# Performance work log

Measured on AMD Instinct MI355X. Metric: run time of the kernel, lower is better.

Reference implementation:

```python
import jax, jax.numpy as jnp
import numpy as np

N = 50000
E = 800000
NUM_KINDS = 100
D_NODE = 64
D_EDGE = 4
D_MSG = 64
L = 3
D_IN = 2 * D_NODE + D_EDGE  # 132


def setup_inputs() -> dict:
    key = jax.random.key(0)
    ks = jax.random.split(key, 20)

    def w(k, shape, fan_in):
        bound = 1.0 / np.sqrt(fan_in)
        return jax.random.uniform(k, shape, jnp.float32, -bound, bound)

    inp = {
        "edge_index": jax.random.randint(ks[0], (2, E), 0, N),
        "node_kind_ids": jax.random.randint(ks[1], (N,), 0, NUM_KINDS),
        "edge_attr": jax.random.normal(ks[2], (E, D_EDGE), jnp.float32),
        # learned params
        "emb": jax.random.normal(ks[3], (NUM_KINDS, D_NODE), jnp.float32),
        # stacked per-layer message MLP params [L, ...]
        "msg_w1": w(ks[4], (L, D_MSG, D_IN), D_IN),
        "msg_b1": w(ks[5], (L, D_MSG), D_IN),
        "msg_w2": w(ks[6], (L, D_MSG, D_MSG), D_MSG),
        "msg_b2": w(ks[7], (L, D_MSG), D_MSG),
        # stacked per-layer GRUCell params (torch layout: [3*d_node, d_in])
        "gru_wih": w(ks[8], (L, 3 * D_NODE, D_MSG), D_NODE),
        "gru_whh": w(ks[9], (L, 3 * D_NODE, D_NODE), D_NODE),
        "gru_bih": w(ks[10], (L, 3 * D_NODE), D_NODE),
        "gru_bhh": w(ks[11], (L, 3 * D_NODE), D_NODE),
        # edge head: Linear(132,64) -> SiLU -> Linear(64,1)
        "head_w1": w(ks[12], (64, D_IN), D_IN),
        "head_b1": w(ks[13], (64,), D_IN),
        "head_w2": w(ks[14], (1, 64), 64),
        "head_b2": w(ks[15], (1,), 64),
    }
    return inp


def reference(edge_index, node_kind_ids, edge_attr, emb,
              msg_w1, msg_b1, msg_w2, msg_b2,
              gru_wih, gru_whh, gru_bih, gru_bhh,
              head_w1, head_b1, head_w2, head_b2):
    src, dst = edge_index[0], edge_index[1]
    h = emb[node_kind_ids]  # [N, d_node]
    n_nodes = h.shape[0]
    for l in range(L):
        x = jnp.concatenate([h[src], h[dst], edge_attr], axis=1)  # [E, 132]
        m = jax.nn.silu(x @ msg_w1[l].T + msg_b1[l]) @ msg_w2[l].T + msg_b2[l]  # [E, d_msg]
        agg = jax.ops.segment_sum(m, dst, num_segments=n_nodes)  # [N, d_msg]
        # torch GRUCell math
        gi = agg @ gru_wih[l].T + gru_bih[l]  # [N, 3*d_node]
        gh = h @ gru_whh[l].T + gru_bhh[l]
        ir, iz, inn = jnp.split(gi, 3, axis=1)
        hr, hz, hn = jnp.split(gh, 3, axis=1)
        r = jax.nn.sigmoid(ir + hr)
        z = jax.nn.sigmoid(iz + hz)
        n = jnp.tanh(inn + r * hn)
        h = (1.0 - z) * n + z * h
    x = jnp.concatenate([h[src], h[dst], edge_attr], axis=1)  # [E, 132]
    logits = (jax.nn.silu(x @ head_w1.T + head_b1) @ head_w2.T + head_b2)[:, 0]
    return jax.nn.sigmoid(logits)  # [E]
```

## Files before the change

### kernel.cpp

```cpp
#include <hip/hip_runtime.h>
#include <hip/hip_bf16.h>


typedef __attribute__((ext_vector_type(8))) short bf16x8;
typedef __attribute__((ext_vector_type(4))) float f32x4;
#define MFMA16(a, b, c) __builtin_amdgcn_mfma_f32_16x16x32_bf16(a, b, c, 0, 0, 0)

#define CHUNK 128
#define XSTRIDE 336
#define MSTRIDE 264
#define HSTRIDE 144
#define SLABSZ 10752
#define HIDSZ  4608

#define WRZST 264
#define WNST  136

__device__ __forceinline__ float fast_sig(float x) { return 1.f / (1.f + __expf(-x)); }
__device__ __forceinline__ float fast_tanh(float x) {
    float ax = fabsf(x);
    float t = __expf(-2.f * ax);
    return copysignf((1.f - t) / (1.f + t), x);
}
__device__ __forceinline__ ushort f2bf(float f) {
    unsigned u = __float_as_uint(f);
    unsigned r = u + 0x7FFF + ((u >> 16) & 1);
    return (ushort)(r >> 16);
}

__global__ void prep_kernel(const float* __restrict__ msg_w1,
                            const float* __restrict__ msg_w2,
                            const float* __restrict__ gru_wih,
                            const float* __restrict__ gru_whh,
                            const float* __restrict__ head_w1,
                            const float* __restrict__ head_w2,
                            ushort* __restrict__ Wb1, ushort* __restrict__ Wb2,
                            ushort* __restrict__ Wh1, ushort* __restrict__ Wh2b,
                            ushort* __restrict__ Wrz, ushort* __restrict__ Wni,
                            ushort* __restrict__ Wnh) {
    int t = blockIdx.x * 256 + threadIdx.x;
    if (t < 30720) {
        int l = t / 10240, r = t % 10240, j = r / 160, k = r % 160;
        Wb1[t] = (k < 132) ? f2bf(msg_w1[l * 8448 + j * 132 + k]) : 0;
        return;
    }
    t -= 30720;
    if (t < 12288) {
        Wb2[t] = f2bf(msg_w2[t]);
        return;
    }
    t -= 12288;
    if (t < 10240) {
        int j = t / 160, k = t % 160;
        Wh1[t] = (k < 132) ? f2bf(head_w1[j * 132 + k]) : 0;
        return;
    }
    t -= 10240;
    if (t < 1024) {
        int j = t >> 6, k = t & 63;
        Wh2b[t] = (j == 0) ? f2bf(head_w2[k]) : 0;
        return;
    }
    t -= 1024;
    if (t < 49152) {
        int l = t / 16384, r = t % 16384, n = r >> 7, k = r & 127;
        float v = (k < 64) ? gru_wih[l * 12288 + n * 64 + k]
                           : gru_whh[l * 12288 + n * 64 + (k - 64)];
        Wrz[t] = f2bf(v);
        return;
    }
    t -= 49152;
    if (t < 12288) {
        int l = t / 4096, r = t % 4096, j = r >> 6, k = r & 63;
        Wni[t] = f2bf(gru_wih[l * 12288 + (128 + j) * 64 + k]);
        return;
    }
    t -= 12288;
    if (t < 12288) {
        int l = t / 4096, r = t % 4096, j = r >> 6, k = r & 63;
        Wnh[t] = f2bf(gru_whh[l * 12288 + (128 + j) * 64 + k]);
    }
}

__global__ void embed_kernel(float* __restrict__ h, ushort* __restrict__ hb,
                             const float* __restrict__ emb,
                             const int* __restrict__ kinds, int N) {
    int t = blockIdx.x * 256 + threadIdx.x;
    if (t >= N * 64) return;
    int node = t >> 6, d = t & 63;
    float v = emb[kinds[node] * 64 + d];
    h[t] = v;
    hb[t] = f2bf(v);
}

__global__ void hist_kernel(const int* __restrict__ dst, int* __restrict__ deg, int E) {
    int e = blockIdx.x * 256 + threadIdx.x;
    if (e < E) atomicAdd(&deg[dst[e]], 1);
}

__global__ void scan_kernel(const int* __restrict__ deg, int* __restrict__ cursor, int N) {
    __shared__ int sums[1024];
    int tid = threadIdx.x;
    int chunk = (N + 1023) >> 10;
    int lo = tid * chunk, hi = min(lo + chunk, N);
    int s = 0;
    for (int i = lo; i < hi; i++) s += deg[i];
    sums[tid] = s;
    __syncthreads();
    for (int off = 1; off < 1024; off <<= 1) {
        int v = (tid >= off) ? sums[tid - off] : 0;
        __syncthreads();
        sums[tid] += v;
        __syncthreads();
    }
    int run = (tid > 0) ? sums[tid - 1] : 0;
    for (int i = lo; i < hi; i++) {
        cursor[i] = run;
        run += deg[i];
    }
}

__global__ void scatter_kernel(const int* __restrict__ src, const int* __restrict__ dst,
                               const float* __restrict__ ea, int* __restrict__ cursor,
                               int* __restrict__ src_s, int* __restrict__ dst_s,
                               ushort* __restrict__ ea_sb, int E) {
    int e = blockIdx.x * 256 + threadIdx.x;
    if (e >= E) return;
    int d = dst[e];
    int p = atomicAdd(&cursor[d], 1);
    src_s[p] = src[e];
    dst_s[p] = d;
    float4 e4 = ((const float4*)ea)[e];
    ushort4 eb;
    eb.x = f2bf(e4.x); eb.y = f2bf(e4.y); eb.z = f2bf(e4.z); eb.w = f2bf(e4.w);
    ((ushort4*)ea_sb)[p] = eb;
}

__global__ __launch_bounds__(256) void edge_msg_mfma(
    const ushort* __restrict__ hb, const int* __restrict__ src_s,
    const int* __restrict__ dst_s, const ushort* __restrict__ ea_sb,
    const ushort* __restrict__ Wb1l, const ushort* __restrict__ Wb2l,
    const float* __restrict__ b1, const float* __restrict__ b2,
    float* __restrict__ agg, int E, int nchunks) {
    __shared__ char lds[4 * SLABSZ + 4 * HIDSZ];
    int tid = threadIdx.x;
    int w = tid >> 6, lane = tid & 63;
    int quad = lane >> 4, nrow = lane & 15;
    char* slab = lds + w * SLABSZ;
    char* hidb = lds + 4 * SLABSZ + w * HIDSZ;

    bf16x8 wf1[4][5], wf2[4][2];
    float b1v[4], b2v[4];
#pragma unroll
    for (int nt = 0; nt < 4; nt++) {
        int n = nt * 16 + nrow;
#pragma unroll
        for (int ks = 0; ks < 5; ks++)
            wf1[nt][ks] = *(const bf16x8*)(Wb1l + n * 160 + ks * 32 + quad * 8);
#pragma unroll
        for (int ks = 0; ks < 2; ks++)
            wf2[nt][ks] = *(const bf16x8*)(Wb2l + n * 64 + ks * 32 + quad * 8);
        b1v[nt] = b1[n];
        b2v[nt] = b2[n];
    }

    for (int chunk = blockIdx.x; chunk < nchunks; chunk += gridDim.x) {
        int ebase = chunk * CHUNK;
        {
            int el = tid >> 1, half = tid & 1;
            int r = el & 31;
            int ec = min(ebase + el, E - 1);
            int node = half ? dst_s[ec] : src_s[ec];
            const float4* hrow = (const float4*)(hb + (size_t)node * 64);
            float4* xw = (float4*)(slab + r * XSTRIDE + half * 128);
#pragma unroll
            for (int i = 0; i < 8; i++) xw[i] = hrow[i];
            if (half == 0) {
                *(uint2*)(slab + r * XSTRIDE + 256) = *(const uint2*)(ea_sb + (size_t)ec * 4);
            } else {
                uint2 z2 = {0u, 0u};
                float4 z4 = {0.f, 0.f, 0.f, 0.f};
                *(uint2*)(slab + r * XSTRIDE + 264) = z2;
                *(float4*)(slab + r * XSTRIDE + 272) = z4;
                *(float4*)(slab + r * XSTRIDE + 288) = z4;
                *(float4*)(slab + r * XSTRIDE + 304) = z4;
            }
        }
        f32x4 acc1[2][4];
#pragma unroll
        for (int mt = 0; mt < 2; mt++)
#pragma unroll
            for (int nt = 0; nt < 4; nt++) {
                f32x4 v;
                v[0] = v[1] = v[2] = v[3] = b1v[nt];
                acc1[mt][nt] = v;
            }
#pragma unroll
        for (int ks = 0; ks < 5; ks++) {
            bf16x8 a0 = *(const bf16x8*)(slab + nrow * XSTRIDE + ks * 64 + quad * 16);
            bf16x8 a1 = *(const bf16x8*)(slab + (16 + nrow) * XSTRIDE + ks * 64 + quad * 16);
#pragma unroll
            for (int nt = 0; nt < 4; nt++) {
                acc1[0][nt] = MFMA16(a0, wf1[nt][ks], acc1[0][nt]);
                acc1[1][nt] = MFMA16(a1, wf1[nt][ks], acc1[1][nt]);
            }
        }
#pragma unroll
        for (int mt = 0; mt < 2; mt++)
#pragma unroll
            for (int nt = 0; nt < 4; nt++)
#pragma unroll
                for (int rg = 0; rg < 4; rg++) {
                    float v = acc1[mt][nt][rg];
                    v = v * fast_sig(v);
                    int rm = mt * 16 + quad * 4 + rg;
                    *(ushort*)(hidb + rm * HSTRIDE + (nt * 16 + nrow) * 2) = f2bf(v);
                }
        f32x4 acc2[2][4];
#pragma unroll
        for (int mt = 0; mt < 2; mt++)
#pragma unroll
            for (int nt = 0; nt < 4; nt++) {
                f32x4 v;
                v[0] = v[1] = v[2] = v[3] = b2v[nt];
                acc2[mt][nt] = v;
            }
#pragma unroll
        for (int ks = 0; ks < 2; ks++) {
            bf16x8 a0 = *(const bf16x8*)(hidb + nrow * HSTRIDE + ks * 64 + quad * 16);
            bf16x8 a1 = *(const bf16x8*)(hidb + (16 + nrow) * HSTRIDE + ks * 64 + quad * 16);
#pragma unroll
            for (int nt = 0; nt < 4; nt++) {
                acc2[0][nt] = MFMA16(a0, wf2[nt][ks], acc2[0][nt]);
                acc2[1][nt] = MFMA16(a1, wf2[nt][ks], acc2[1][nt]);
            }
        }
#pragma unroll
        for (int mt = 0; mt < 2; mt++)
#pragma unroll
            for (int nt = 0; nt < 4; nt++)
#pragma unroll
                for (int rg = 0; rg < 4; rg++) {
                    int rm = mt * 16 + quad * 4 + rg;
                    *(float*)(slab + rm * MSTRIDE + (nt * 16 + nrow) * 4) = acc2[mt][nt][rg];
                }
        {
            int e32 = ebase + w * 32;
            int dmy = dst_s[min(e32 + (lane & 31), E - 1)];
            int limit = min(32, E - e32);
            int nx = __shfl_down(dmy, 1);
            bool tl = ((lane & 31) == 31) || (dmy != nx);
            unsigned long long tm = __ballot(tl);
            float run = 0.f;
#pragma unroll
            for (int i = 0; i < 32; i++) {
                if (i < limit) {
                    run += *(const float*)(slab + i * MSTRIDE + lane * 4);
                    if (((tm >> i) & 1ull) || (i + 1 == limit)) {
                        int di = __shfl(dmy, i);
                        unsafeAtomicAdd(&agg[(size_t)di * 64 + lane], run);
                        run = 0.f;
                    }
                }
            }
        }
    }
}

__global__ __launch_bounds__(256) void head_mfma(
    const ushort* __restrict__ hb, const int* __restrict__ src,
    const int* __restrict__ dst, const float* __restrict__ ea,
    const ushort* __restrict__ Wh1, const ushort* __restrict__ Wh2b,
    const float* __restrict__ hb1, const float* __restrict__ hb2p,
    float* __restrict__ out, int E, int nchunks) {
    __shared__ char lds[4 * SLABSZ + 4 * HIDSZ];
    int tid = threadIdx.x;
    int w = tid >> 6, lane = tid & 63;
    int quad = lane >> 4, nrow = lane & 15;
    char* slab = lds + w * SLABSZ;
    char* hidb = lds + 4 * SLABSZ + w * HIDSZ;

    bf16x8 wf1[4][5], wh2[2];
    float b1v[4];
#pragma unroll
    for (int nt = 0; nt < 4; nt++) {
        int n = nt * 16 + nrow;
#pragma unroll
        for (int ks = 0; ks < 5; ks++)
            wf1[nt][ks] = *(const bf16x8*)(Wh1 + n * 160 + ks * 32 + quad * 8);
        b1v[nt] = hb1[n];
    }
#pragma unroll
    for (int ks = 0; ks < 2; ks++)
        wh2[ks] = *(const bf16x8*)(Wh2b + nrow * 64 + ks * 32 + quad * 8);
    float hb2 = hb2p[0];

    for (int chunk = blockIdx.x; chunk < nchunks; chunk += gridDim.x) {
        int ebase = chunk * CHUNK;
        {
            int el = tid >> 1, half = tid & 1;
            int r = el & 31;
            int ec = min(ebase + el, E - 1);
            int node = half ? dst[ec] : src[ec];
            const float4* hrow = (const float4*)(hb + (size_t)node * 64);
            float4* xw = (float4*)(slab + r * XSTRIDE + half * 128);
#pragma unroll
            for (int i = 0; i < 8; i++) xw[i] = hrow[i];
            if (half == 0) {
                float4 e4 = ((const float4*)ea)[ec];
                ushort4 eb;
                eb.x = f2bf(e4.x); eb.y = f2bf(e4.y); eb.z = f2bf(e4.z); eb.w = f2bf(e4.w);
                *(ushort4*)(slab + r * XSTRIDE + 256) = eb;
            } else {
                uint2 z2 = {0u, 0u};
                float4 z4 = {0.f, 0.f, 0.f, 0.f};
                *(uint2*)(slab + r * XSTRIDE + 264) = z2;
                *(float4*)(slab + r * XSTRIDE + 272) = z4;
                *(float4*)(slab + r * XSTRIDE + 288) = z4;
                *(float4*)(slab + r * XSTRIDE + 304) = z4;
            }
        }
        f32x4 acc1[2][4];
#pragma unroll
        for (int mt = 0; mt < 2; mt++)
#pragma unroll
            for (int nt = 0; nt < 4; nt++) {
                f32x4 v;
                v[0] = v[1] = v[2] = v[3] = b1v[nt];
                acc1[mt][nt] = v;
            }
#pragma unroll
        for (int ks = 0; ks < 5; ks++) {
            bf16x8 a0 = *(const bf16x8*)(slab + nrow * XSTRIDE + ks * 64 + quad * 16);
            bf16x8 a1 = *(const bf16x8*)(slab + (16 + nrow) * XSTRIDE + ks * 64 + quad * 16);
#pragma unroll
            for (int nt = 0; nt < 4; nt++) {
                acc1[0][nt] = MFMA16(a0, wf1[nt][ks], acc1[0][nt]);
                acc1[1][nt] = MFMA16(a1, wf1[nt][ks], acc1[1][nt]);
            }
        }
#pragma unroll
        for (int mt = 0; mt < 2; mt++)
#pragma unroll
            for (int nt = 0; nt < 4; nt++)
#pragma unroll
                for (int rg = 0; rg < 4; rg++) {
                    float v = acc1[mt][nt][rg];
                    v = v * fast_sig(v);
                    int rm = mt * 16 + quad * 4 + rg;
                    *(ushort*)(hidb + rm * HSTRIDE + (nt * 16 + nrow) * 2) = f2bf(v);
                }
        f32x4 acc3[2];
#pragma unroll
        for (int mt = 0; mt < 2; mt++) {
            f32x4 v;
            v[0] = v[1] = v[2] = v[3] = 0.f;
            acc3[mt] = v;
        }
#pragma unroll
        for (int ks = 0; ks < 2; ks++) {
            bf16x8 a0 = *(const bf16x8*)(hidb + nrow * HSTRIDE + ks * 64 + quad * 16);
            bf16x8 a1 = *(const bf16x8*)(hidb + (16 + nrow) * HSTRIDE + ks * 64 + quad * 16);
            acc3[0] = MFMA16(a0, wh2[ks], acc3[0]);
            acc3[1] = MFMA16(a1, wh2[ks], acc3[1]);
        }
        if (nrow == 0) {
#pragma unroll
            for (int mt = 0; mt < 2; mt++)
#pragma unroll
                for (int rg = 0; rg < 4; rg++) {
                    int e = ebase + w * 32 + mt * 16 + quad * 4 + rg;
                    if (e < E) out[e] = fast_sig(acc3[mt][rg] + hb2);
                }
        }
    }
}

__device__ __forceinline__ bf16x8 aggfrag(const float* __restrict__ row, int off) {
    float4 f0 = *(const float4*)(row + off);
    float4 f1 = *(const float4*)(row + off + 4);
    bf16x8 r;
    r[0] = (short)f2bf(f0.x); r[1] = (short)f2bf(f0.y);
    r[2] = (short)f2bf(f0.z); r[3] = (short)f2bf(f0.w);
    r[4] = (short)f2bf(f1.x); r[5] = (short)f2bf(f1.y);
    r[6] = (short)f2bf(f1.z); r[7] = (short)f2bf(f1.w);
    return r;
}

__global__ __launch_bounds__(256) void gru_mfma(
    float* __restrict__ h, ushort* __restrict__ hb, const float* __restrict__ agg,
    const ushort* __restrict__ Wrzg, const ushort* __restrict__ Wnig,
    const ushort* __restrict__ Wnhg,
    const float* __restrict__ bih, const float* __restrict__ bhh, int N) {
    __shared__ char lds[128 * WRZST + 2 * 64 * WNST];
    int tid = threadIdx.x, w = tid >> 6, lane = tid & 63;
    int quad = lane >> 4, nrow = lane & 15;
    char* wrz = lds;
    char* wni = lds + 128 * WRZST;
    char* wnh = wni + 64 * WNST;

    {
        int r = tid >> 1, half = tid & 1;
        const uint4* g = (const uint4*)(Wrzg + r * 128 + half * 64);
        uint4* d = (uint4*)(wrz + r * WRZST + half * 128);
#pragma unroll
        for (int i = 0; i < 8; i++) d[i] = g[i];
        if (tid < 128) {
            const uint4* g2 = (const uint4*)(Wnig + (tid >> 1) * 64 + (tid & 1) * 32);
            uint4* d2 = (uint4*)(wni + (tid >> 1) * WNST + (tid & 1) * 64);
#pragma unroll
            for (int i = 0; i < 4; i++) d2[i] = g2[i];
        } else {
            int t2 = tid - 128;
            const uint4* g2 = (const uint4*)(Wnhg + (t2 >> 1) * 64 + (t2 & 1) * 32);
            uint4* d2 = (uint4*)(wnh + (t2 >> 1) * WNST + (t2 & 1) * 64);
#pragma unroll
            for (int i = 0; i < 4; i++) d2[i] = g2[i];
        }
    }
    __syncthreads();

    int nb0 = blockIdx.x * 128 + w * 32;
    if (nb0 >= N) return;

    float brz[8], bi[4], bhv[4];
#pragma unroll
    for (int nt = 0; nt < 8; nt++) brz[nt] = bih[nt * 16 + nrow] + bhh[nt * 16 + nrow];
#pragma unroll
    for (int nt = 0; nt < 4; nt++) {
        bi[nt] = bih[128 + nt * 16 + nrow];
        bhv[nt] = bhh[128 + nt * 16 + nrow];
    }

    int n0 = min(nb0 + nrow, N - 1);
    int n1 = min(nb0 + 16 + nrow, N - 1);
    const float* ag0 = agg + (size_t)n0 * 64;
    const float* ag1 = agg + (size_t)n1 * 64;
    const ushort* hb0 = hb + (size_t)n0 * 64;
    const ushort* hb1 = hb + (size_t)n1 * 64;

    f32x4 accrz[2][8], acci[2][4], acch[2][4];
#pragma unroll
    for (int nt = 0; nt < 8; nt++) {
        f32x4 v; v[0] = v[1] = v[2] = v[3] = brz[nt];
        accrz[0][nt] = v; accrz[1][nt] = v;
    }
#pragma unroll
    for (int nt = 0; nt < 4; nt++) {
        f32x4 vi; vi[0] = vi[1] = vi[2] = vi[3] = bi[nt];
        acci[0][nt] = vi; acci[1][nt] = vi;
        f32x4 vh; vh[0] = vh[1] = vh[2] = vh[3] = bhv[nt];
        acch[0][nt] = vh; acch[1][nt] = vh;
    }

#pragma unroll
    for (int ks = 0; ks < 4; ks++) {
        bf16x8 a0, a1;
        if (ks < 2) {
            a0 = aggfrag(ag0, ks * 32 + quad * 8);
            a1 = aggfrag(ag1, ks * 32 + quad * 8);
        } else {
            a0 = *(const bf16x8*)(hb0 + (ks - 2) * 32 + quad * 8);
            a1 = *(const bf16x8*)(hb1 + (ks - 2) * 32 + quad * 8);
        }
#pragma unroll
        for (int nt = 0; nt < 8; nt++) {
            bf16x8 b = *(const bf16x8*)(wrz + (nt * 16 + nrow) * WRZST + ks * 64 + quad * 16);
            accrz[0][nt] = MFMA16(a0, b, accrz[0][nt]);
            accrz[1][nt] = MFMA16(a1, b, accrz[1][nt]);
        }
        if (ks < 2) {
#pragma unroll
            for (int nt = 0; nt < 4; nt++) {
                bf16x8 b = *(const bf16x8*)(wni + (nt * 16 + nrow) * WNST + ks * 64 + quad * 16);
                acci[0][nt] = MFMA16(a0, b, acci[0][nt]);
                acci[1][nt] = MFMA16(a1, b, acci[1][nt]);
            }
        } else {
#pragma unroll
            for (int nt = 0; nt < 4; nt++) {
                bf16x8 b = *(const bf16x8*)(wnh + (nt * 16 + nrow) * WNST + (ks - 2) * 64 + quad * 16);
                acch[0][nt] = MFMA16(a0, b, acch[0][nt]);
                acch[1][nt] = MFMA16(a1, b, acch[1][nt]);
            }
        }
    }

#pragma unroll
    for (int mt = 0; mt < 2; mt++)
#pragma unroll
        for (int nt = 0; nt < 4; nt++)
#pragma unroll
            for (int rg = 0; rg < 4; rg++) {
                int node = nb0 + mt * 16 + quad * 4 + rg;
                if (node < N) {
                    int col = nt * 16 + nrow;
                    float r = fast_sig(accrz[mt][nt][rg]);
                    float z = fast_sig(accrz[mt][nt + 4][rg]);
                    float nn = fast_tanh(acci[mt][nt][rg] + r * acch[mt][nt][rg]);
                    size_t idx = (size_t)node * 64 + col;
                    float ho = h[idx];
                    float hnew = (1.f - z) * nn + z * ho;
                    h[idx] = hnew;
                    hb[idx] = f2bf(hnew);
                }
            }
}

extern "C" void kernel_launch(void* const* d_in, const int* in_sizes, int n_in,
                              void* d_out, int out_size, void* d_ws, size_t ws_size,
                              hipStream_t stream) {
    const int* edge_index = (const int*)d_in[0];
    int E = in_sizes[0] / 2;
    const int* src = edge_index;
    const int* dst = edge_index + E;
    const int* kinds = (const int*)d_in[1];
    int N = in_sizes[1];
    const float* edge_attr = (const float*)d_in[2];
    const float* emb = (const float*)d_in[3];
    const float* msg_w1 = (const float*)d_in[4];
    const float* msg_b1 = (const float*)d_in[5];
    const float* msg_w2 = (const float*)d_in[6];
    const float* msg_b2 = (const float*)d_in[7];
    const float* gru_wih = (const float*)d_in[8];
    const float* gru_whh = (const float*)d_in[9];
    const float* gru_bih = (const float*)d_in[10];
    const float* gru_bhh = (const float*)d_in[11];
    const float* head_w1 = (const float*)d_in[12];
    const float* head_b1 = (const float*)d_in[13];
    const float* head_w2 = (const float*)d_in[14];
    const float* head_b2 = (const float*)d_in[15];
    float* out = (float*)d_out;

    char* p = (char*)d_ws;
    float* h = (float*)p;        p += (size_t)N * 64 * 4;
    float* agg = (float*)p;      p += (size_t)N * 64 * 4;
    int* deg = (int*)p;          p += (size_t)N * 4;
    int* cursor = (int*)p;       p += (size_t)N * 4;
    int* src_s = (int*)p;        p += (size_t)E * 4;
    int* dst_s = (int*)p;        p += (size_t)E * 4;
    ushort* hb = (ushort*)p;     p += (size_t)N * 64 * 2;
    ushort* Wb1 = (ushort*)p;    p += 30720 * 2;
    ushort* Wb2 = (ushort*)p;    p += 12288 * 2;
    ushort* Wh1 = (ushort*)p;    p += 10240 * 2;
    ushort* Wh2b = (ushort*)p;   p += 1024 * 2;
    ushort* Wrz = (ushort*)p;    p += 49152 * 2;
    ushort* Wni = (ushort*)p;    p += 12288 * 2;
    ushort* Wnh = (ushort*)p;    p += 12288 * 2;
    ushort* ea_sb = (ushort*)p;  p += (size_t)E * 4 * 2;

    int nchunks = (E + CHUNK - 1) / CHUNK;

    prep_kernel<<<500, 256, 0, stream>>>(msg_w1, msg_w2, gru_wih, gru_whh, head_w1,
                                         head_w2, Wb1, Wb2, Wh1, Wh2b, Wrz, Wni, Wnh);
    embed_kernel<<<(N * 64 + 255) / 256, 256, 0, stream>>>(h, hb, emb, kinds, N);

    hipMemsetAsync(deg, 0, (size_t)N * sizeof(int), stream);
    hist_kernel<<<(E + 255) / 256, 256, 0, stream>>>(dst, deg, E);
    scan_kernel<<<1, 1024, 0, stream>>>(deg, cursor, N);
    scatter_kernel<<<(E + 255) / 256, 256, 0, stream>>>(src, dst, edge_attr, cursor,
                                                        src_s, dst_s, ea_sb, E);

    for (int l = 0; l < 3; l++) {
        hipMemsetAsync(agg, 0, (size_t)N * 64 * sizeof(float), stream);
        edge_msg_mfma<<<512, 256, 0, stream>>>(
            hb, src_s, dst_s, ea_sb,
            Wb1 + l * 10240, Wb2 + l * 4096,
            msg_b1 + l * 64, msg_b2 + l * 64, agg, E, nchunks);
        gru_mfma<<<(N + 127) / 128, 256, 0, stream>>>(
            h, hb, agg, Wrz + l * 16384, Wni + l * 4096, Wnh + l * 4096,
            gru_bih + l * 192, gru_bhh + l * 192, N);
    }
    head_mfma<<<512, 256, 0, stream>>>(hb, src, dst, edge_attr, Wh1, Wh2b,
                                       head_b1, head_b2, out, E, nchunks);
}
```

Measured before the change: 686.3 us.

## Load gathered node rows directly into MFMA registers, skipping the LDS staging slab

The edge message and head kernels now gather h[src]/h[dst] rows and edge attributes straight into MFMA operand registers, using the transposed product (W as A, X as B), instead of staging a padded slab in LDS. The hidden activations go to a smaller XOR-swizzled LDS buffer and are packed to bf16 with v_cvt_pk_bf16_f32. LDS use per block shrinks, which should let more blocks run per CU. The segmented atomic reduction is split into groups of 8 rows, which may issue more atomics.

```diff
diff --git a/kernel.cpp b/kernel.cpp
--- a/kernel.cpp
+++ b/kernel.cpp
@@ -7,11 +7,9 @@
 #define MFMA16(a, b, c) __builtin_amdgcn_mfma_f32_16x16x32_bf16(a, b, c, 0, 0, 0)
 
 #define CHUNK 128
-#define XSTRIDE 336
 #define MSTRIDE 264
-#define HSTRIDE 144
-#define SLABSZ 10752
-#define HIDSZ  4608
+#define EBUF 8448
+#define HIDB 4096
 
 #define WRZST 264
 #define WNST  136
@@ -26,6 +24,11 @@
     unsigned u = __float_as_uint(f);
     unsigned r = u + 0x7FFF + ((u >> 16) & 1);
     return (ushort)(r >> 16);
+}
+__device__ __forceinline__ unsigned pkbf2(float a, float b) {
+    unsigned r;
+    asm("v_cvt_pk_bf16_f32 %0, %1, %2" : "=v"(r) : "v"(a), "v"(b));
+    return r;
 }
 
 __global__ void prep_kernel(const float* __restrict__ msg_w1,
@@ -142,15 +145,15 @@
     const ushort* __restrict__ Wb1l, const ushort* __restrict__ Wb2l,
     const float* __restrict__ b1, const float* __restrict__ b2,
     float* __restrict__ agg, int E, int nchunks) {
-    __shared__ char lds[4 * SLABSZ + 4 * HIDSZ];
+    __shared__ char lds[4 * EBUF];
     int tid = threadIdx.x;
     int w = tid >> 6, lane = tid & 63;
     int quad = lane >> 4, nrow = lane & 15;
-    char* slab = lds + w * SLABSZ;
-    char* hidb = lds + 4 * SLABSZ + w * HIDSZ;
+    char* buf = lds + w * EBUF;
 
     bf16x8 wf1[4][5], wf2[4][2];
-    float b1v[4], b2v[4];
+    f32x4 b1q[4];
+    float b2v[4];
 #pragma unroll
     for (int nt = 0; nt < 4; nt++) {
         int n = nt * 16 + nrow;
@@ -160,81 +163,100 @@
 #pragma unroll
         for (int ks = 0; ks < 2; ks++)
             wf2[nt][ks] = *(const bf16x8*)(Wb2l + n * 64 + ks * 32 + quad * 8);
-        b1v[nt] = b1[n];
+        b1q[nt] = *(const f32x4*)(b1 + nt * 16 + quad * 4);
         b2v[nt] = b2[n];
     }
 
     for (int chunk = blockIdx.x; chunk < nchunks; chunk += gridDim.x) {
-        int ebase = chunk * CHUNK;
+        int ebase = chunk * CHUNK + w * 32;
+        int e0 = min(ebase + nrow, E - 1);
+        int e1 = min(ebase + 16 + nrow, E - 1);
+        int s0 = src_s[e0], s1 = src_s[e1];
+        int d0 = dst_s[e0], d1 = dst_s[e1];
+
+        bf16x8 x0[5], x1[5];
         {
-            int el = tid >> 1, half = tid & 1;
-            int r = el & 31;
-            int ec = min(ebase + el, E - 1);
-            int node = half ? dst_s[ec] : src_s[ec];
-            const float4* hrow = (const float4*)(hb + (size_t)node * 64);
-            float4* xw = (float4*)(slab + r * XSTRIDE + half * 128);
-#pragma unroll
-            for (int i = 0; i < 8; i++) xw[i] = hrow[i];
-            if (half == 0) {
-                *(uint2*)(slab + r * XSTRIDE + 256) = *(const uint2*)(ea_sb + (size_t)ec * 4);
-            } else {
-                uint2 z2 = {0u, 0u};
-                float4 z4 = {0.f, 0.f, 0.f, 0.f};
-                *(uint2*)(slab + r * XSTRIDE + 264) = z2;
-                *(float4*)(slab + r * XSTRIDE + 272) = z4;
-                *(float4*)(slab + r * XSTRIDE + 288) = z4;
-                *(float4*)(slab + r * XSTRIDE + 304) = z4;
-            }
-        }
-        f32x4 acc1[2][4];
+            const ushort* p = hb + (size_t)s0 * 64 + quad * 8;
+            x0[0] = *(const bf16x8*)p;
+            x0[1] = *(const bf16x8*)(p + 32);
+            p = hb + (size_t)d0 * 64 + quad * 8;
+            x0[2] = *(const bf16x8*)p;
+            x0[3] = *(const bf16x8*)(p + 32);
+            p = hb + (size_t)s1 * 64 + quad * 8;
+            x1[0] = *(const bf16x8*)p;
+            x1[1] = *(const bf16x8*)(p + 32);
+            p = hb + (size_t)d1 * 64 + quad * 8;
+            x1[2] = *(const bf16x8*)p;
+            x1[3] = *(const bf16x8*)(p + 32);
+            bf16x8 z = {0, 0, 0, 0, 0, 0, 0, 0};
+            x0[4] = z;
+            x1[4] = z;
+            if (quad == 0) {
+                ushort4 v0 = *(const ushort4*)(ea_sb + (size_t)e0 * 4);
+                ushort4 v1 = *(const ushort4*)(ea_sb + (size_t)e1 * 4);
+                x0[4][0] = (short)v0.x; x0[4][1] = (short)v0.y;
+                x0[4][2] = (short)v0.z; x0[4][3] = (short)v0.w;
+                x1[4][0] = (short)v1.x; x1[4][1] = (short)v1.y;
+                x1[4][2] = (short)v1.z; x1[4][3] = (short)v1.w;
+            }
+        }
+
+        f32x4 acc[4][2];
+#pragma unroll
+        for (int nt = 0; nt < 4; nt++) {
+            acc[nt][0] = b1q[nt];
+            acc[nt][1] = b1q[nt];
+        }
+#pragma unroll
+        for (int ks = 0; ks < 5; ks++)
+#pragma unroll
+            for (int nt = 0; nt < 4; nt++) {
+                acc[nt][0] = MFMA16(wf1[nt][ks], x0[ks], acc[nt][0]);
+                acc[nt][1] = MFMA16(wf1[nt][ks], x1[ks], acc[nt][1]);
+            }
+
+#pragma unroll
+        for (int nt = 0; nt < 4; nt++)
+#pragma unroll
+            for (int et = 0; et < 2; et++) {
+                f32x4 a = acc[nt][et];
+                float v0 = a[0] * fast_sig(a[0]);
+                float v1 = a[1] * fast_sig(a[1]);
+                float v2 = a[2] * fast_sig(a[2]);
+                float v3 = a[3] * fast_sig(a[3]);
+                int er = et * 16 + nrow;
+                int off = er * 128 + ((nt * 32 + quad * 8) ^ ((er & 7) << 4));
+                uint2 pk;
+                pk.x = pkbf2(v0, v1);
+                pk.y = pkbf2(v2, v3);
+                *(uint2*)(buf + off) = pk;
+            }
+
+        bf16x8 ha[2][2];
 #pragma unroll
         for (int mt = 0; mt < 2; mt++)
 #pragma unroll
+            for (int ks = 0; ks < 2; ks++) {
+                int er = mt * 16 + nrow;
+                ha[mt][ks] = *(const bf16x8*)(
+                    buf + er * 128 + ((ks * 64 + quad * 16) ^ ((er & 7) << 4)));
+            }
+        f32x4 acc2[2][4];
+#pragma unroll
+        for (int nt = 0; nt < 4; nt++) {
+            f32x4 v;
+            v[0] = v[1] = v[2] = v[3] = b2v[nt];
+            acc2[0][nt] = v;
+            acc2[1][nt] = v;
+        }
+#pragma unroll
+        for (int ks = 0; ks < 2; ks++)
+#pragma unroll
             for (int nt = 0; nt < 4; nt++) {
-                f32x4 v;
-                v[0] = v[1] = v[2] = v[3] = b1v[nt];
-                acc1[mt][nt] = v;
-            }
-#pragma unroll
-        for (int ks = 0; ks < 5; ks++) {
-            bf16x8 a0 = *(const bf16x8*)(slab + nrow * XSTRIDE + ks * 64 + quad * 16);
-            bf16x8 a1 = *(const bf16x8*)(slab + (16 + nrow) * XSTRIDE + ks * 64 + quad * 16);
-#pragma unroll
-            for (int nt = 0; nt < 4; nt++) {
-                acc1[0][nt] = MFMA16(a0, wf1[nt][ks], acc1[0][nt]);
-                acc1[1][nt] = MFMA16(a1, wf1[nt][ks], acc1[1][nt]);
-            }
-        }
-#pragma unroll
-        for (int mt = 0; mt < 2; mt++)
-#pragma unroll
-            for (int nt = 0; nt < 4; nt++)
-#pragma unroll
-                for (int rg = 0; rg < 4; rg++) {
-                    float v = acc1[mt][nt][rg];
-                    v = v * fast_sig(v);
-                    int rm = mt * 16 + quad * 4 + rg;
-                    *(ushort*)(hidb + rm * HSTRIDE + (nt * 16 + nrow) * 2) = f2bf(v);
-                }
-        f32x4 acc2[2][4];
-#pragma unroll
-        for (int mt = 0; mt < 2; mt++)
-#pragma unroll
-            for (int nt = 0; nt < 4; nt++) {
-                f32x4 v;
-                v[0] = v[1] = v[2] = v[3] = b2v[nt];
-                acc2[mt][nt] = v;
-            }
-#pragma unroll
-        for (int ks = 0; ks < 2; ks++) {
-            bf16x8 a0 = *(const bf16x8*)(hidb + nrow * HSTRIDE + ks * 64 + quad * 16);
-            bf16x8 a1 = *(const bf16x8*)(hidb + (16 + nrow) * HSTRIDE + ks * 64 + quad * 16);
-#pragma unroll
-            for (int nt = 0; nt < 4; nt++) {
-                acc2[0][nt] = MFMA16(a0, wf2[nt][ks], acc2[0][nt]);
-                acc2[1][nt] = MFMA16(a1, wf2[nt][ks], acc2[1][nt]);
-            }
-        }
+                acc2[0][nt] = MFMA16(ha[0][ks], wf2[nt][ks], acc2[0][nt]);
+                acc2[1][nt] = MFMA16(ha[1][ks], wf2[nt][ks], acc2[1][nt]);
+            }
+
 #pragma unroll
         for (int mt = 0; mt < 2; mt++)
 #pragma unroll
@@ -242,24 +264,29 @@
 #pragma unroll
                 for (int rg = 0; rg < 4; rg++) {
                     int rm = mt * 16 + quad * 4 + rg;
-                    *(float*)(slab + rm * MSTRIDE + (nt * 16 + nrow) * 4) = acc2[mt][nt][rg];
+                    *(float*)(buf + rm * MSTRIDE + (nt * 16 + nrow) * 4) =
+                        acc2[mt][nt][rg];
                 }
+
         {
-            int e32 = ebase + w * 32;
-            int dmy = dst_s[min(e32 + (lane & 31), E - 1)];
-            int limit = min(32, E - e32);
+            int dmy = (lane & 16) ? d1 : d0;
+            int limit = min(32, E - ebase);
             int nx = __shfl_down(dmy, 1);
             bool tl = ((lane & 31) == 31) || (dmy != nx);
             unsigned long long tm = __ballot(tl);
-            float run = 0.f;
-#pragma unroll
-            for (int i = 0; i < 32; i++) {
-                if (i < limit) {
-                    run += *(const float*)(slab + i * MSTRIDE + lane * 4);
-                    if (((tm >> i) & 1ull) || (i + 1 == limit)) {
-                        int di = __shfl(dmy, i);
-                        unsafeAtomicAdd(&agg[(size_t)di * 64 + lane], run);
-                        run = 0.f;
+#pragma unroll
+            for (int g = 0; g < 4; g++) {
+                float run = 0.f;
+#pragma unroll
+                for (int i = 0; i < 8; i++) {
+                    int idx = g * 8 + i;
+                    if (idx < limit) {
+                        run += *(const float*)(buf + idx * MSTRIDE + lane * 4);
+                        if (((tm >> idx) & 1ull) || (i == 7) || (idx + 1 == limit)) {
+                            int di = __shfl(dmy, idx);
+                            unsafeAtomicAdd(&agg[(size_t)di * 64 + lane], run);
+                            run = 0.f;
+                        }
                     }
                 }
             }
@@ -273,22 +300,21 @@
     const ushort* __restrict__ Wh1, const ushort* __restrict__ Wh2b,
     const float* __restrict__ hb1, const float* __restrict__ hb2p,
     float* __restrict__ out, int E, int nchunks) {
-    __shared__ char lds[4 * SLABSZ + 4 * HIDSZ];
+    __shared__ char lds[4 * HIDB];
     int tid = threadIdx.x;
     int w = tid >> 6, lane = tid & 63;
     int quad = lane >> 4, nrow = lane & 15;
-    char* slab = lds + w * SLABSZ;
-    char* hidb = lds + 4 * SLABSZ + w * HIDSZ;
+    char* buf = lds + w * HIDB;
 
     bf16x8 wf1[4][5], wh2[2];
-    float b1v[4];
+    f32x4 b1q[4];
 #pragma unroll
     for (int nt = 0; nt < 4; nt++) {
         int n = nt * 16 + nrow;
 #pragma unroll
         for (int ks = 0; ks < 5; ks++)
             wf1[nt][ks] = *(const bf16x8*)(Wh1 + n * 160 + ks * 32 + quad * 8);
-        b1v[nt] = hb1[n];
+        b1q[nt] = *(const f32x4*)(hb1 + nt * 16 + quad * 4);
     }
 #pragma unroll
     for (int ks = 0; ks < 2; ks++)
@@ -296,60 +322,79 @@
     float hb2 = hb2p[0];
 
     for (int chunk = blockIdx.x; chunk < nchunks; chunk += gridDim.x) {
-        int ebase = chunk * CHUNK;
+        int ebase = chunk * CHUNK + w * 32;
+        int e0 = min(ebase + nrow, E - 1);
+        int e1 = min(ebase + 16 + nrow, E - 1);
+        int s0 = src[e0], s1 = src[e1];
+        int d0 = dst[e0], d1 = dst[e1];
+
+        bf16x8 x0[5], x1[5];
         {
-            int el = tid >> 1, half = tid & 1;
-            int r = el & 31;
-            int ec = min(ebase + el, E - 1);
-            int node = half ? dst[ec] : src[ec];
-            const float4* hrow = (const float4*)(hb + (size_t)node * 64);
-            float4* xw = (float4*)(slab + r * XSTRIDE + half * 128);
-#pragma unroll
-            for (int i = 0; i < 8; i++) xw[i] = hrow[i];
-            if (half == 0) {
-                float4 e4 = ((const float4*)ea)[ec];
-                ushort4 eb;
-                eb.x = f2bf(e4.x); eb.y = f2bf(e4.y); eb.z = f2bf(e4.z); eb.w = f2bf(e4.w);
-                *(ushort4*)(slab + r * XSTRIDE + 256) = eb;
-            } else {
-                uint2 z2 = {0u, 0u};
-                float4 z4 = {0.f, 0.f, 0.f, 0.f};
-                *(uint2*)(slab + r * XSTRIDE + 264) = z2;
-                *(float4*)(slab + r * XSTRIDE + 272) = z4;
-                *(float4*)(slab + r * XSTRIDE + 288) = z4;
-                *(float4*)(slab + r * XSTRIDE + 304) = z4;
-            }
-        }
-        f32x4 acc1[2][4];
+            const ushort* p = hb + (size_t)s0 * 64 + quad * 8;
+            x0[0] = *(const bf16x8*)p;
+            x0[1] = *(const bf16x8*)(p + 32);
+            p = hb + (size_t)d0 * 64 + quad * 8;
+            x0[2] = *(const bf16x8*)p;
+            x0[3] = *(const bf16x8*)(p + 32);
+            p = hb + (size_t)s1 * 64 + quad * 8;
+            x1[0] = *(const bf16x8*)p;
+            x1[1] = *(const bf16x8*)(p + 32);
+            p = hb + (size_t)d1 * 64 + quad * 8;
+            x1[2] = *(const bf16x8*)p;
+            x1[3] = *(const bf16x8*)(p + 32);
+            bf16x8 z = {0, 0, 0, 0, 0, 0, 0, 0};
+            x0[4] = z;
+            x1[4] = z;
+            if (quad == 0) {
+                float4 q0 = ((const float4*)ea)[e0];
+                float4 q1 = ((const float4*)ea)[e1];
+                x0[4][0] = (short)f2bf(q0.x); x0[4][1] = (short)f2bf(q0.y);
+                x0[4][2] = (short)f2bf(q0.z); x0[4][3] = (short)f2bf(q0.w);
+                x1[4][0] = (short)f2bf(q1.x); x1[4][1] = (short)f2bf(q1.y);
+                x1[4][2] = (short)f2bf(q1.z); x1[4][3] = (short)f2bf(q1.w);
+            }
+        }
+
+        f32x4 acc[4][2];
+#pragma unroll
+        for (int nt = 0; nt < 4; nt++) {
+            acc[nt][0] = b1q[nt];
+            acc[nt][1] = b1q[nt];
+        }
+#pragma unroll
+        for (int ks = 0; ks < 5; ks++)
+#pragma unroll
+            for (int nt = 0; nt < 4; nt++) {
+                acc[nt][0] = MFMA16(wf1[nt][ks], x0[ks], acc[nt][0]);
+                acc[nt][1] = MFMA16(wf1[nt][ks], x1[ks], acc[nt][1]);
+            }
+
+#pragma unroll
+        for (int nt = 0; nt < 4; nt++)
+#pragma unroll
+            for (int et = 0; et < 2; et++) {
+                f32x4 a = acc[nt][et];
+                float v0 = a[0] * fast_sig(a[0]);
+                float v1 = a[1] * fast_sig(a[1]);
+                float v2 = a[2] * fast_sig(a[2]);
+                float v3 = a[3] * fast_sig(a[3]);
+                int er = et * 16 + nrow;
+                int off = er * 128 + ((nt * 32 + quad * 8) ^ ((er & 7) << 4));
+                uint2 pk;
+                pk.x = pkbf2(v0, v1);
+                pk.y = pkbf2(v2, v3);
+                *(uint2*)(buf + off) = pk;
+            }
+
+        bf16x8 ha[2][2];
 #pragma unroll
         for (int mt = 0; mt < 2; mt++)
 #pragma unroll
-            for (int nt = 0; nt < 4; nt++) {
-                f32x4 v;
-                v[0] = v[1] = v[2] = v[3] = b1v[nt];
-                acc1[mt][nt] = v;
-            }
-#pragma unroll
-        for (int ks = 0; ks < 5; ks++) {
-            bf16x8 a0 = *(const bf16x8*)(slab + nrow * XSTRIDE + ks * 64 + quad * 16);
-            bf16x8 a1 = *(const bf16x8*)(slab + (16 + nrow) * XSTRIDE + ks * 64 + quad * 16);
-#pragma unroll
-            for (int nt = 0; nt < 4; nt++) {
-                acc1[0][nt] = MFMA16(a0, wf1[nt][ks], acc1[0][nt]);
-                acc1[1][nt] = MFMA16(a1, wf1[nt][ks], acc1[1][nt]);
-            }
-        }
-#pragma unroll
-        for (int mt = 0; mt < 2; mt++)
-#pragma unroll
-            for (int nt = 0; nt < 4; nt++)
-#pragma unroll
-                for (int rg = 0; rg < 4; rg++) {
-                    float v = acc1[mt][nt][rg];
-                    v = v * fast_sig(v);
-                    int rm = mt * 16 + quad * 4 + rg;
-                    *(ushort*)(hidb + rm * HSTRIDE + (nt * 16 + nrow) * 2) = f2bf(v);
-                }
+            for (int ks = 0; ks < 2; ks++) {
+                int er = mt * 16 + nrow;
+                ha[mt][ks] = *(const bf16x8*)(
+                    buf + er * 128 + ((ks * 64 + quad * 16) ^ ((er & 7) << 4)));
+            }
         f32x4 acc3[2];
 #pragma unroll
         for (int mt = 0; mt < 2; mt++) {
@@ -359,17 +404,15 @@
         }
 #pragma unroll
         for (int ks = 0; ks < 2; ks++) {
-            bf16x8 a0 = *(const bf16x8*)(hidb + nrow * HSTRIDE + ks * 64 + quad * 16);
-            bf16x8 a1 = *(const bf16x8*)(hidb + (16 + nrow) * HSTRIDE + ks * 64 + quad * 16);
-            acc3[0] = MFMA16(a0, wh2[ks], acc3[0]);
-            acc3[1] = MFMA16(a1, wh2[ks], acc3[1]);
+            acc3[0] = MFMA16(ha[0][ks], wh2[ks], acc3[0]);
+            acc3[1] = MFMA16(ha[1][ks], wh2[ks], acc3[1]);
         }
         if (nrow == 0) {
 #pragma unroll
             for (int mt = 0; mt < 2; mt++)
 #pragma unroll
                 for (int rg = 0; rg < 4; rg++) {
-                    int e = ebase + w * 32 + mt * 16 + quad * 4 + rg;
+                    int e = ebase + mt * 16 + quad * 4 + rg;
                     if (e < E) out[e] = fast_sig(acc3[mt][rg] + hb2);
                 }
         }
```

Measured after the change: 800.7 us. +16.7%, slower.
